# Kernel tuning notes

Hardware: AMD Instinct MI355X
Metric: run time of the kernel (lower is better)

Reference implementation:

```python
import jax, jax.numpy as jnp
import numpy as np

N = 10000
E = 320000
D_IN = 256
D_OUT = 256
EPS = 0.2  # initial value of trainable eps


def setup_inputs() -> dict:
    key = jax.random.key(0)
    ks = jax.random.split(key, 7)
    x = jax.random.normal(ks[0], (N, D_IN), dtype=jnp.float32)
    edge_index = jax.random.randint(ks[1], (2, E), 0, N, dtype=jnp.int64)
    # MLP params (Linear(in,out) -> ReLU -> Linear(out,out)), Kaiming-ish scale
    w1 = jax.random.normal(ks[2], (D_IN, D_OUT), dtype=jnp.float32) / np.sqrt(D_IN)
    b1 = jnp.zeros((D_OUT,), dtype=jnp.float32)
    w2 = jax.random.normal(ks[3], (D_OUT, D_OUT), dtype=jnp.float32) / np.sqrt(D_OUT)
    b2 = jnp.zeros((D_OUT,), dtype=jnp.float32)
    eps = jnp.float32(EPS)
    return {"x": x, "edge_index": edge_index, "w1": w1, "b1": b1,
            "w2": w2, "b2": b2, "eps": eps}


def reference(x, edge_index, w1, b1, w2, b2, eps):
    src, dst = edge_index[0], edge_index[1]
    # GIN sum aggregation: agg[i] = sum_{(j->i) in E} x[j]
    msgs = x[src]  # [E, D_IN] gather
    agg = jax.ops.segment_sum(msgs, dst, num_segments=N)  # [N, D_IN] scatter-add
    h = (1.0 + eps) * x + agg
    # 2-layer MLP
    h = jax.nn.relu(h @ w1 + b1)
    out = h @ w2 + b2
    return out
```

## Files before the change

kernel.cpp:

```cpp
#include <hip/hip_runtime.h>

#define NN 10000
#define NE 320000
#define CAP 96

typedef __bf16 bf16x8 __attribute__((ext_vector_type(8)));
typedef float f32x4 __attribute__((ext_vector_type(4)));
typedef unsigned short us8 __attribute__((ext_vector_type(8)));

static __device__ __forceinline__ unsigned short f2bf(float f) {
  union { float fv; unsigned u; } v; v.fv = f;
  unsigned r = v.u + 0x7FFFu + ((v.u >> 16) & 1u);
  return (unsigned short)(r >> 16);
}
static __device__ __forceinline__ float bf2f(unsigned short b) {
  union { unsigned u; float f; } v; v.u = ((unsigned)b) << 16;
  return v.f;
}


__global__ __launch_bounds__(256) void conv_k(const float* __restrict__ x,
                                              const float* __restrict__ w1,
                                              const float* __restrict__ w2,
                                              ushort4* __restrict__ xb4,
                                              unsigned short* __restrict__ w1t,
                                              unsigned short* __restrict__ w2t,
                                              int* __restrict__ cnt) {
  __shared__ unsigned short sh[64][72];
  int bid = blockIdx.x, tid = threadIdx.x;
  if (bid < 2500) {
    int t = bid * 256 + tid;
    if (t < 10240) cnt[t] = 0;
    float4 v = reinterpret_cast<const float4*>(x)[t];
    ushort4 o;
    o.x = f2bf(v.x); o.y = f2bf(v.y); o.z = f2bf(v.z); o.w = f2bf(v.w);
    xb4[t] = o;
  } else {
    int b2 = bid - 2500;
    const float* w = (b2 & 16) ? w2 : w1;
    unsigned short* wt = (b2 & 16) ? w2t : w1t;
    int tile = b2 & 15;
    int ki0 = (tile >> 2) * 64, ni0 = (tile & 3) * 64;
    int r = tid >> 4, c = tid & 15;
#pragma unroll
    for (int rr = r; rr < 64; rr += 16) {
      float4 v = *reinterpret_cast<const float4*>(&w[(ki0 + rr) * 256 + ni0 + c * 4]);
      ushort4 o;
      o.x = f2bf(v.x); o.y = f2bf(v.y); o.z = f2bf(v.z); o.w = f2bf(v.w);
      *reinterpret_cast<ushort4*>(&sh[rr][c * 4]) = o;
    }
    __syncthreads();
    int n = tid >> 3, c8 = tid & 7;
#pragma unroll
    for (int nn = n; nn < 64; nn += 32) {
      us8 o;
#pragma unroll
      for (int j = 0; j < 8; ++j) o[j] = sh[c8 * 8 + j][nn];
      *reinterpret_cast<us8*>(&wt[(ni0 + nn) * 256 + ki0 + c8 * 8]) = o;
    }
  }
}


__global__ __launch_bounds__(256) void fill_k(const int* __restrict__ ei,
                                              int* __restrict__ cnt,
                                              int* __restrict__ bucket) {
  int e = (blockIdx.x * 256 + threadIdx.x) * 4;
  if (e < NE) {
    int4 s = *reinterpret_cast<const int4*>(&ei[e]);
    int4 d = *reinterpret_cast<const int4*>(&ei[NE + e]);
    int p;
    p = atomicAdd(&cnt[d.x], 1); if (p < CAP) bucket[d.x * CAP + p] = s.x;
    p = atomicAdd(&cnt[d.y], 1); if (p < CAP) bucket[d.y * CAP + p] = s.y;
    p = atomicAdd(&cnt[d.z], 1); if (p < CAP) bucket[d.z * CAP + p] = s.z;
    p = atomicAdd(&cnt[d.w], 1); if (p < CAP) bucket[d.w * CAP + p] = s.w;
  }
}


__global__ __launch_bounds__(256) void agg_k(const us8* __restrict__ xb8,
                                             const int* __restrict__ cnt,
                                             const int* __restrict__ bucket,
                                             const float* __restrict__ epsp,
                                             unsigned short* __restrict__ hb) {
  __shared__ float part[2][256];
  int tid = threadIdx.x;
  int wave = tid >> 6;
  int slot = wave >> 1;
  int p = wave & 1;
  int node = blockIdx.x * 2 + slot;
  int lane = tid & 63;
  int half = lane >> 5, off = lane & 31;
  float e1 = 1.0f + epsp[0];

  float a[8];
  if (p == 0) {
    us8 sv = xb8[node * 32 + off];
    float selfw = half ? 0.0f : e1;
#pragma unroll
    for (int j = 0; j < 8; ++j) a[j] = bf2f(sv[j]) * selfw;
  } else {
#pragma unroll
    for (int j = 0; j < 8; ++j) a[j] = 0.0f;
  }

  int n = min(cnt[node], CAP);
  int n0 = ((n + 4) >> 3) << 2;
  int s = p ? n0 : 0;
  int m = (p ? n : n0) - s;
  const int4* bp4 = reinterpret_cast<const int4*>(bucket + node * CAP + s);
  int4 ia = bp4[0], ib = bp4[1];
  int k = 0;
  while (k + 8 <= m) {
    int4 na = bp4[(k >> 2) + 2];
    int4 nb = bp4[(k >> 2) + 3];
    int r0 = half ? ia.y : ia.x;
    int r1 = half ? ia.w : ia.z;
    int r2 = half ? ib.y : ib.x;
    int r3 = half ? ib.w : ib.z;
    us8 v0 = xb8[r0 * 32 + off];
    us8 v1 = xb8[r1 * 32 + off];
    us8 v2 = xb8[r2 * 32 + off];
    us8 v3 = xb8[r3 * 32 + off];
#pragma unroll
    for (int j = 0; j < 8; ++j)
      a[j] += (bf2f(v0[j]) + bf2f(v1[j])) + (bf2f(v2[j]) + bf2f(v3[j]));
    ia = na; ib = nb; k += 8;
  }
  int tl = m - k;
#pragma unroll
  for (int q = 0; q < 4; ++q) {
    int idx = (q == 0) ? (half ? ia.y : ia.x)
            : (q == 1) ? (half ? ia.w : ia.z)
            : (q == 2) ? (half ? ib.y : ib.x)
                       : (half ? ib.w : ib.z);
    if (2 * q + half < tl) {
      us8 v = xb8[idx * 32 + off];
#pragma unroll
      for (int j = 0; j < 8; ++j) a[j] += bf2f(v[j]);
    }
  }
#pragma unroll
  for (int j = 0; j < 8; ++j) a[j] += __shfl_xor(a[j], 32);
  if (p == 1 && half == 0) {
#pragma unroll
    for (int j = 0; j < 8; ++j) part[slot][j * 32 + off] = a[j];
  }
  __syncthreads();
  if (p == 0 && half == 0) {
    us8 o;
#pragma unroll
    for (int j = 0; j < 8; ++j) o[j] = f2bf(a[j] + part[slot][j * 32 + off]);
    *reinterpret_cast<us8*>(&hb[node * 256 + off * 8]) = o;
  }
}


__global__ __launch_bounds__(256) void mlp_k(const unsigned short* __restrict__ hb,
                                             const unsigned short* __restrict__ w1t,
                                             const float* __restrict__ b1,
                                             const unsigned short* __restrict__ w2t,
                                             const float* __restrict__ b2,
                                             float* __restrict__ out) {
  __shared__ unsigned short As[32][264];
  __shared__ unsigned short Bs[256][72];
  int m0 = blockIdx.x * 32;
  int tid = threadIdx.x;
  int lane = tid & 63, wave = tid >> 6;
  int waveM = wave & 1, waveN = wave >> 1;
  int l15 = lane & 15, g = lane >> 4;
#pragma unroll
  for (int i = 0; i < 4; ++i) {
    int c = tid + i * 256;
    int r = c >> 5, cc = c & 31;
    int4 v = (m0 + r < NN)
                 ? *reinterpret_cast<const int4*>(&hb[(m0 + r) * 256 + cc * 8])
                 : make_int4(0, 0, 0, 0);
    *reinterpret_cast<int4*>(&As[r][cc * 8]) = v;
  }
  float bias1[8], bias2[8];
#pragma unroll
  for (int ni = 0; ni < 8; ++ni) {
    int col = waveN * 128 + ni * 16 + l15;
    bias1[ni] = b1[col];
    bias2[ni] = b2[col];
  }
  f32x4 acc[8];
#pragma unroll
  for (int ni = 0; ni < 8; ++ni) acc[ni] = f32x4{0.f, 0.f, 0.f, 0.f};
  for (int k0 = 0; k0 < 256; k0 += 64) {
#pragma unroll
    for (int i = 0; i < 8; ++i) {
      int c = tid + i * 256;
      int n = c >> 3, kc = c & 7;
      *reinterpret_cast<int4*>(&Bs[n][kc * 8]) =
          *reinterpret_cast<const int4*>(&w1t[n * 256 + k0 + kc * 8]);
    }
    __syncthreads();
#pragma unroll
    for (int kk = 0; kk < 2; ++kk) {
      bf16x8 af = *reinterpret_cast<const bf16x8*>(
          &As[waveM * 16 + l15][k0 + kk * 32 + g * 8]);
#pragma unroll
      for (int ni = 0; ni < 8; ++ni) {
        bf16x8 bfr = *reinterpret_cast<const bf16x8*>(
            &Bs[waveN * 128 + ni * 16 + l15][kk * 32 + g * 8]);
        acc[ni] = __builtin_amdgcn_mfma_f32_16x16x32_bf16(af, bfr, acc[ni], 0, 0, 0);
      }
    }
    __syncthreads();
  }
#pragma unroll
  for (int ni = 0; ni < 8; ++ni) {
    int col = waveN * 128 + ni * 16 + l15;
#pragma unroll
    for (int r = 0; r < 4; ++r) {
      int row = waveM * 16 + g * 4 + r;
      As[row][col] = f2bf(fmaxf(acc[ni][r] + bias1[ni], 0.f));
    }
    acc[ni] = f32x4{0.f, 0.f, 0.f, 0.f};
  }
  for (int k0 = 0; k0 < 256; k0 += 64) {
#pragma unroll
    for (int i = 0; i < 8; ++i) {
      int c = tid + i * 256;
      int n = c >> 3, kc = c & 7;
      *reinterpret_cast<int4*>(&Bs[n][kc * 8]) =
          *reinterpret_cast<const int4*>(&w2t[n * 256 + k0 + kc * 8]);
    }
    __syncthreads();
#pragma unroll
    for (int kk = 0; kk < 2; ++kk) {
      bf16x8 af = *reinterpret_cast<const bf16x8*>(
          &As[waveM * 16 + l15][k0 + kk * 32 + g * 8]);
#pragma unroll
      for (int ni = 0; ni < 8; ++ni) {
        bf16x8 bfr = *reinterpret_cast<const bf16x8*>(
            &Bs[waveN * 128 + ni * 16 + l15][kk * 32 + g * 8]);
        acc[ni] = __builtin_amdgcn_mfma_f32_16x16x32_bf16(af, bfr, acc[ni], 0, 0, 0);
      }
    }
    __syncthreads();
  }
#pragma unroll
  for (int ni = 0; ni < 8; ++ni) {
    int col = waveN * 128 + ni * 16 + l15;
#pragma unroll
    for (int r = 0; r < 4; ++r) {
      int row = m0 + waveM * 16 + g * 4 + r;
      if (row < NN) out[row * 256 + col] = acc[ni][r] + bias2[ni];
    }
  }
}


extern "C" void kernel_launch(void* const* d_in, const int* in_sizes, int n_in,
                              void* d_out, int out_size, void* d_ws, size_t ws_size,
                              hipStream_t stream) {
  const float* x = (const float*)d_in[0];
  const int* ei = (const int*)d_in[1];
  const float* w1 = (const float*)d_in[2];
  const float* b1 = (const float*)d_in[3];
  const float* w2 = (const float*)d_in[4];
  const float* b2 = (const float*)d_in[5];
  const float* eps = (const float*)d_in[6];
  float* out = (float*)d_out;

  int* cnt = (int*)d_ws;
  int* bucket = cnt + 10240;
  unsigned short* xb = (unsigned short*)(bucket + NN * CAP + 32);
  unsigned short* w1t = xb + NN * 256;
  unsigned short* w2t = w1t + 65536;
  unsigned short* hb = w2t + 65536;

  conv_k<<<2532, 256, 0, stream>>>(x, w1, w2, (ushort4*)xb, w1t, w2t, cnt);
  fill_k<<<(NE / 4 + 255) / 256, 256, 0, stream>>>(ei, cnt, bucket);
  agg_k<<<NN / 2, 256, 0, stream>>>((const us8*)xb, cnt, bucket, eps, hb);
  mlp_k<<<(NN + 31) / 32, 256, 0, stream>>>(hb, w1t, b1, w2t, b2, out);
}
```

Before: 64.07 us.

## Fuse conversion and bucket fill into one prep kernel, deepen gather unroll

Merges the x/weight bf16 conversion kernel and the edge-bucket fill kernel into a single grid-stride prep kernel. The count array is now zeroed with a memset issued before it. This removes one kernel launch and lets the atomic fill overlap with the conversion traffic. The aggregation loop now issues 8 neighbour gathers per iteration instead of 4 to keep more loads in flight, with a wider tail and larger bucket padding. The trade-offs are an extra memset launch and more registers per thread in the aggregation kernel.

```diff
diff --git a/kernel.cpp b/kernel.cpp
--- a/kernel.cpp
+++ b/kernel.cpp
@@ -3,6 +3,8 @@
 #define NN 10000
 #define NE 320000
 #define CAP 96
+#define K1BLK 1024
+#define K1TOT (K1BLK * 256)
 
 typedef __bf16 bf16x8 __attribute__((ext_vector_type(8)));
 typedef float f32x4 __attribute__((ext_vector_type(4)));
@@ -19,54 +21,21 @@
 }
 
 
-__global__ __launch_bounds__(256) void conv_k(const float* __restrict__ x,
+__global__ __launch_bounds__(256) void prep_k(const float* __restrict__ x,
+                                              const int* __restrict__ ei,
                                               const float* __restrict__ w1,
                                               const float* __restrict__ w2,
                                               ushort4* __restrict__ xb4,
                                               unsigned short* __restrict__ w1t,
                                               unsigned short* __restrict__ w2t,
-                                              int* __restrict__ cnt) {
+                                              int* __restrict__ cnt,
+                                              int* __restrict__ bucket) {
   __shared__ unsigned short sh[64][72];
   int bid = blockIdx.x, tid = threadIdx.x;
-  if (bid < 2500) {
-    int t = bid * 256 + tid;
-    if (t < 10240) cnt[t] = 0;
-    float4 v = reinterpret_cast<const float4*>(x)[t];
-    ushort4 o;
-    o.x = f2bf(v.x); o.y = f2bf(v.y); o.z = f2bf(v.z); o.w = f2bf(v.w);
-    xb4[t] = o;
-  } else {
-    int b2 = bid - 2500;
-    const float* w = (b2 & 16) ? w2 : w1;
-    unsigned short* wt = (b2 & 16) ? w2t : w1t;
-    int tile = b2 & 15;
-    int ki0 = (tile >> 2) * 64, ni0 = (tile & 3) * 64;
-    int r = tid >> 4, c = tid & 15;
-#pragma unroll
-    for (int rr = r; rr < 64; rr += 16) {
-      float4 v = *reinterpret_cast<const float4*>(&w[(ki0 + rr) * 256 + ni0 + c * 4]);
-      ushort4 o;
-      o.x = f2bf(v.x); o.y = f2bf(v.y); o.z = f2bf(v.z); o.w = f2bf(v.w);
-      *reinterpret_cast<ushort4*>(&sh[rr][c * 4]) = o;
-    }
-    __syncthreads();
-    int n = tid >> 3, c8 = tid & 7;
-#pragma unroll
-    for (int nn = n; nn < 64; nn += 32) {
-      us8 o;
-#pragma unroll
-      for (int j = 0; j < 8; ++j) o[j] = sh[c8 * 8 + j][nn];
-      *reinterpret_cast<us8*>(&wt[(ni0 + nn) * 256 + ki0 + c8 * 8]) = o;
-    }
-  }
-}
-
-
-__global__ __launch_bounds__(256) void fill_k(const int* __restrict__ ei,
-                                              int* __restrict__ cnt,
-                                              int* __restrict__ bucket) {
-  int e = (blockIdx.x * 256 + threadIdx.x) * 4;
-  if (e < NE) {
+  int gtid = bid * 256 + tid;
+
+  if (gtid < NE / 4) {
+    int e = gtid * 4;
     int4 s = *reinterpret_cast<const int4*>(&ei[e]);
     int4 d = *reinterpret_cast<const int4*>(&ei[NE + e]);
     int p;
@@ -74,6 +43,38 @@
     p = atomicAdd(&cnt[d.y], 1); if (p < CAP) bucket[d.y * CAP + p] = s.y;
     p = atomicAdd(&cnt[d.z], 1); if (p < CAP) bucket[d.z * CAP + p] = s.z;
     p = atomicAdd(&cnt[d.w], 1); if (p < CAP) bucket[d.w * CAP + p] = s.w;
+  }
+
+  for (int t = gtid; t < 640000; t += K1TOT) {
+    float4 v = reinterpret_cast<const float4*>(x)[t];
+    ushort4 o;
+    o.x = f2bf(v.x); o.y = f2bf(v.y); o.z = f2bf(v.z); o.w = f2bf(v.w);
+    xb4[t] = o;
+  }
+
+  if (bid >= 512 && bid < 544) {
+    int b2 = bid - 512;
+    const float* w = (b2 & 16) ? w2 : w1;
+    unsigned short* wt = (b2 & 16) ? w2t : w1t;
+    int tile = b2 & 15;
+    int ki0 = (tile >> 2) * 64, ni0 = (tile & 3) * 64;
+    int r = tid >> 4, c = tid & 15;
+#pragma unroll
+    for (int rr = r; rr < 64; rr += 16) {
+      float4 v = *reinterpret_cast<const float4*>(&w[(ki0 + rr) * 256 + ni0 + c * 4]);
+      ushort4 o;
+      o.x = f2bf(v.x); o.y = f2bf(v.y); o.z = f2bf(v.z); o.w = f2bf(v.w);
+      *reinterpret_cast<ushort4*>(&sh[rr][c * 4]) = o;
+    }
+    __syncthreads();
+    int n = tid >> 3, c8 = tid & 7;
+#pragma unroll
+    for (int nn = n; nn < 64; nn += 32) {
+      us8 o;
+#pragma unroll
+      for (int j = 0; j < 8; ++j) o[j] = sh[c8 * 8 + j][nn];
+      *reinterpret_cast<us8*>(&wt[(ni0 + nn) * 256 + ki0 + c8 * 8]) = o;
+    }
   }
 }
 
@@ -109,36 +110,44 @@
   int s = p ? n0 : 0;
   int m = (p ? n : n0) - s;
   const int4* bp4 = reinterpret_cast<const int4*>(bucket + node * CAP + s);
-  int4 ia = bp4[0], ib = bp4[1];
+  int4 ia = bp4[0], ib = bp4[1], ic = bp4[2], id = bp4[3];
   int k = 0;
-  while (k + 8 <= m) {
-    int4 na = bp4[(k >> 2) + 2];
-    int4 nb = bp4[(k >> 2) + 3];
-    int r0 = half ? ia.y : ia.x;
-    int r1 = half ? ia.w : ia.z;
-    int r2 = half ? ib.y : ib.x;
-    int r3 = half ? ib.w : ib.z;
+  while (k + 16 <= m) {
+    int base = (k >> 2) + 4;
+    int4 na = bp4[base], nb = bp4[base + 1];
+    int4 nc = bp4[base + 2], nd = bp4[base + 3];
+    int r0 = half ? ia.y : ia.x, r1 = half ? ia.w : ia.z;
+    int r2 = half ? ib.y : ib.x, r3 = half ? ib.w : ib.z;
+    int r4 = half ? ic.y : ic.x, r5 = half ? ic.w : ic.z;
+    int r6 = half ? id.y : id.x, r7 = half ? id.w : id.z;
     us8 v0 = xb8[r0 * 32 + off];
     us8 v1 = xb8[r1 * 32 + off];
     us8 v2 = xb8[r2 * 32 + off];
     us8 v3 = xb8[r3 * 32 + off];
+    us8 v4 = xb8[r4 * 32 + off];
+    us8 v5 = xb8[r5 * 32 + off];
+    us8 v6 = xb8[r6 * 32 + off];
+    us8 v7 = xb8[r7 * 32 + off];
 #pragma unroll
     for (int j = 0; j < 8; ++j)
-      a[j] += (bf2f(v0[j]) + bf2f(v1[j])) + (bf2f(v2[j]) + bf2f(v3[j]));
-    ia = na; ib = nb; k += 8;
+      a[j] += ((bf2f(v0[j]) + bf2f(v1[j])) + (bf2f(v2[j]) + bf2f(v3[j]))) +
+              ((bf2f(v4[j]) + bf2f(v5[j])) + (bf2f(v6[j]) + bf2f(v7[j])));
+    ia = na; ib = nb; ic = nc; id = nd; k += 16;
   }
   int tl = m - k;
-#pragma unroll
-  for (int q = 0; q < 4; ++q) {
-    int idx = (q == 0) ? (half ? ia.y : ia.x)
-            : (q == 1) ? (half ? ia.w : ia.z)
-            : (q == 2) ? (half ? ib.y : ib.x)
-                       : (half ? ib.w : ib.z);
-    if (2 * q + half < tl) {
-      us8 v = xb8[idx * 32 + off];
-#pragma unroll
-      for (int j = 0; j < 8; ++j) a[j] += bf2f(v[j]);
-    }
+  {
+    int r0 = half ? ia.y : ia.x, r1 = half ? ia.w : ia.z;
+    int r2 = half ? ib.y : ib.x, r3 = half ? ib.w : ib.z;
+    int r4 = half ? ic.y : ic.x, r5 = half ? ic.w : ic.z;
+    int r6 = half ? id.y : id.x, r7 = half ? id.w : id.z;
+#define TAILQ(q, rq)                                        \
+    if (2 * q + half < tl) {                                \
+      us8 v = xb8[rq * 32 + off];                           \
+      _Pragma("unroll") for (int j = 0; j < 8; ++j) a[j] += bf2f(v[j]); \
+    }
+    TAILQ(0, r0) TAILQ(1, r1) TAILQ(2, r2) TAILQ(3, r3)
+    TAILQ(4, r4) TAILQ(5, r5) TAILQ(6, r6) TAILQ(7, r7)
+#undef TAILQ
   }
 #pragma unroll
   for (int j = 0; j < 8; ++j) a[j] += __shfl_xor(a[j], 32);
@@ -268,13 +277,14 @@
 
   int* cnt = (int*)d_ws;
   int* bucket = cnt + 10240;
-  unsigned short* xb = (unsigned short*)(bucket + NN * CAP + 32);
+  unsigned short* xb = (unsigned short*)(bucket + NN * CAP + 64);
   unsigned short* w1t = xb + NN * 256;
   unsigned short* w2t = w1t + 65536;
   unsigned short* hb = w2t + 65536;
 
-  conv_k<<<2532, 256, 0, stream>>>(x, w1, w2, (ushort4*)xb, w1t, w2t, cnt);
-  fill_k<<<(NE / 4 + 255) / 256, 256, 0, stream>>>(ei, cnt, bucket);
+  hipMemsetAsync(cnt, 0, 10240 * sizeof(int), stream);
+  prep_k<<<K1BLK, 256, 0, stream>>>(x, ei, w1, w2, (ushort4*)xb, w1t, w2t,
+                                    cnt, bucket);
   agg_k<<<NN / 2, 256, 0, stream>>>((const us8*)xb, cnt, bucket, eps, hb);
   mlp_k<<<(NN + 31) / 32, 256, 0, stream>>>(hb, w1t, b1, w2t, b2, out);
 }
```

Result: slower. 71.41 us (+11.5%).

## Fuse neighbor aggregation into MLP kernel with 1024-thread blocks and register-prefetched weights

Applied to the files above, without the earlier changes.

Merges the aggregation and MLP kernels into one 1024-thread kernel. Each of the 16 waves aggregates two node rows straight into the shared A tile, so the bf16 intermediate h no longer goes through global memory and one launch is dropped. The MLP is split across 16 waves, each computing a 16x32 output tile, and the next weight chunk is prefetched into registers while the current chunk's MFMAs run. The cost is that aggregation now uses one wave per node instead of two, so per-node parallelism drops and degree imbalance inside a block can stall the GEMM phase. The large blocks also limit occupancy and scheduling flexibility.

```diff
diff --git a/kernel.cpp b/kernel.cpp
--- a/kernel.cpp
+++ b/kernel.cpp
@@ -78,173 +78,156 @@
 }
 
 
-__global__ __launch_bounds__(256) void agg_k(const us8* __restrict__ xb8,
-                                             const int* __restrict__ cnt,
-                                             const int* __restrict__ bucket,
-                                             const float* __restrict__ epsp,
-                                             unsigned short* __restrict__ hb) {
-  __shared__ float part[2][256];
-  int tid = threadIdx.x;
-  int wave = tid >> 6;
-  int slot = wave >> 1;
-  int p = wave & 1;
-  int node = blockIdx.x * 2 + slot;
-  int lane = tid & 63;
-  int half = lane >> 5, off = lane & 31;
-  float e1 = 1.0f + epsp[0];
-
-  float a[8];
-  if (p == 0) {
-    us8 sv = xb8[node * 32 + off];
-    float selfw = half ? 0.0f : e1;
-#pragma unroll
-    for (int j = 0; j < 8; ++j) a[j] = bf2f(sv[j]) * selfw;
-  } else {
-#pragma unroll
-    for (int j = 0; j < 8; ++j) a[j] = 0.0f;
-  }
-
-  int n = min(cnt[node], CAP);
-  int n0 = ((n + 4) >> 3) << 2;
-  int s = p ? n0 : 0;
-  int m = (p ? n : n0) - s;
-  const int4* bp4 = reinterpret_cast<const int4*>(bucket + node * CAP + s);
-  int4 ia = bp4[0], ib = bp4[1];
-  int k = 0;
-  while (k + 8 <= m) {
-    int4 na = bp4[(k >> 2) + 2];
-    int4 nb = bp4[(k >> 2) + 3];
-    int r0 = half ? ia.y : ia.x;
-    int r1 = half ? ia.w : ia.z;
-    int r2 = half ? ib.y : ib.x;
-    int r3 = half ? ib.w : ib.z;
-    us8 v0 = xb8[r0 * 32 + off];
-    us8 v1 = xb8[r1 * 32 + off];
-    us8 v2 = xb8[r2 * 32 + off];
-    us8 v3 = xb8[r3 * 32 + off];
-#pragma unroll
-    for (int j = 0; j < 8; ++j)
-      a[j] += (bf2f(v0[j]) + bf2f(v1[j])) + (bf2f(v2[j]) + bf2f(v3[j]));
-    ia = na; ib = nb; k += 8;
-  }
-  int tl = m - k;
-#pragma unroll
-  for (int q = 0; q < 4; ++q) {
-    int idx = (q == 0) ? (half ? ia.y : ia.x)
-            : (q == 1) ? (half ? ia.w : ia.z)
-            : (q == 2) ? (half ? ib.y : ib.x)
-                       : (half ? ib.w : ib.z);
-    if (2 * q + half < tl) {
-      us8 v = xb8[idx * 32 + off];
-#pragma unroll
-      for (int j = 0; j < 8; ++j) a[j] += bf2f(v[j]);
-    }
-  }
-#pragma unroll
-  for (int j = 0; j < 8; ++j) a[j] += __shfl_xor(a[j], 32);
-  if (p == 1 && half == 0) {
-#pragma unroll
-    for (int j = 0; j < 8; ++j) part[slot][j * 32 + off] = a[j];
-  }
-  __syncthreads();
-  if (p == 0 && half == 0) {
-    us8 o;
-#pragma unroll
-    for (int j = 0; j < 8; ++j) o[j] = f2bf(a[j] + part[slot][j * 32 + off]);
-    *reinterpret_cast<us8*>(&hb[node * 256 + off * 8]) = o;
-  }
-}
-
-
-__global__ __launch_bounds__(256) void mlp_k(const unsigned short* __restrict__ hb,
-                                             const unsigned short* __restrict__ w1t,
-                                             const float* __restrict__ b1,
-                                             const unsigned short* __restrict__ w2t,
-                                             const float* __restrict__ b2,
-                                             float* __restrict__ out) {
+__global__ __launch_bounds__(1024, 4) void fused_k(
+    const us8* __restrict__ xb8, const int* __restrict__ cnt,
+    const int* __restrict__ bucket, const float* __restrict__ epsp,
+    const unsigned short* __restrict__ w1t, const float* __restrict__ b1,
+    const unsigned short* __restrict__ w2t, const float* __restrict__ b2,
+    float* __restrict__ out) {
   __shared__ unsigned short As[32][264];
   __shared__ unsigned short Bs[256][72];
   int m0 = blockIdx.x * 32;
-  int tid = threadIdx.x;
-  int lane = tid & 63, wave = tid >> 6;
+  int tid = threadIdx.x, lane = tid & 63, wave = tid >> 6;
+  int half = lane >> 5, off = lane & 31;
+  float e1 = 1.0f + epsp[0];
+
+#pragma unroll
+  for (int which = 0; which < 2; ++which) {
+    int row = wave * 2 + which;
+    int node = m0 + row;
+    float a[8];
+    if (node < NN) {
+      us8 sv = xb8[node * 32 + off];
+      float selfw = half ? 0.0f : e1;
+#pragma unroll
+      for (int j = 0; j < 8; ++j) a[j] = bf2f(sv[j]) * selfw;
+      int n = min(cnt[node], CAP);
+      const int4* bp4 = reinterpret_cast<const int4*>(bucket + node * CAP);
+      int4 ia = bp4[0], ib = bp4[1];
+      int k = 0;
+      while (k + 8 <= n) {
+        int4 na = bp4[(k >> 2) + 2];
+        int4 nb = bp4[(k >> 2) + 3];
+        int r0 = half ? ia.y : ia.x;
+        int r1 = half ? ia.w : ia.z;
+        int r2 = half ? ib.y : ib.x;
+        int r3 = half ? ib.w : ib.z;
+        us8 v0 = xb8[r0 * 32 + off];
+        us8 v1 = xb8[r1 * 32 + off];
+        us8 v2 = xb8[r2 * 32 + off];
+        us8 v3 = xb8[r3 * 32 + off];
+#pragma unroll
+        for (int j = 0; j < 8; ++j)
+          a[j] += (bf2f(v0[j]) + bf2f(v1[j])) + (bf2f(v2[j]) + bf2f(v3[j]));
+        ia = na; ib = nb; k += 8;
+      }
+      int tl = n - k;
+#pragma unroll
+      for (int q = 0; q < 4; ++q) {
+        int idx = (q == 0) ? (half ? ia.y : ia.x)
+                : (q == 1) ? (half ? ia.w : ia.z)
+                : (q == 2) ? (half ? ib.y : ib.x)
+                           : (half ? ib.w : ib.z);
+        if (2 * q + half < tl) {
+          us8 v = xb8[idx * 32 + off];
+#pragma unroll
+          for (int j = 0; j < 8; ++j) a[j] += bf2f(v[j]);
+        }
+      }
+#pragma unroll
+      for (int j = 0; j < 8; ++j) a[j] += __shfl_xor(a[j], 32);
+    } else {
+#pragma unroll
+      for (int j = 0; j < 8; ++j) a[j] = 0.0f;
+    }
+    if (half == 0) {
+      us8 o;
+#pragma unroll
+      for (int j = 0; j < 8; ++j) o[j] = f2bf(a[j]);
+      *reinterpret_cast<us8*>(&As[row][off * 8]) = o;
+    }
+  }
+
   int waveM = wave & 1, waveN = wave >> 1;
   int l15 = lane & 15, g = lane >> 4;
-#pragma unroll
-  for (int i = 0; i < 4; ++i) {
-    int c = tid + i * 256;
-    int r = c >> 5, cc = c & 31;
-    int4 v = (m0 + r < NN)
-                 ? *reinterpret_cast<const int4*>(&hb[(m0 + r) * 256 + cc * 8])
-                 : make_int4(0, 0, 0, 0);
-    *reinterpret_cast<int4*>(&As[r][cc * 8]) = v;
-  }
-  float bias1[8], bias2[8];
-#pragma unroll
-  for (int ni = 0; ni < 8; ++ni) {
-    int col = waveN * 128 + ni * 16 + l15;
+  float bias1[2], bias2[2];
+#pragma unroll
+  for (int ni = 0; ni < 2; ++ni) {
+    int col = waveN * 32 + ni * 16 + l15;
     bias1[ni] = b1[col];
     bias2[ni] = b2[col];
   }
-  f32x4 acc[8];
-#pragma unroll
-  for (int ni = 0; ni < 8; ++ni) acc[ni] = f32x4{0.f, 0.f, 0.f, 0.f};
-  for (int k0 = 0; k0 < 256; k0 += 64) {
-#pragma unroll
-    for (int i = 0; i < 8; ++i) {
-      int c = tid + i * 256;
-      int n = c >> 3, kc = c & 7;
-      *reinterpret_cast<int4*>(&Bs[n][kc * 8]) =
-          *reinterpret_cast<const int4*>(&w1t[n * 256 + k0 + kc * 8]);
-    }
-    __syncthreads();
+
+  int4 rv[2];
+#pragma unroll
+  for (int i = 0; i < 2; ++i) {
+    int c = tid + i * 1024;
+    int n = c >> 3, kc = c & 7;
+    rv[i] = *reinterpret_cast<const int4*>(&w1t[n * 256 + kc * 8]);
+  }
+#pragma unroll
+  for (int i = 0; i < 2; ++i) {
+    int c = tid + i * 1024;
+    int n = c >> 3, kc = c & 7;
+    *reinterpret_cast<int4*>(&Bs[n][kc * 8]) = rv[i];
+  }
+  __syncthreads();
+
+  f32x4 acc[2];
+  acc[0] = f32x4{0.f, 0.f, 0.f, 0.f};
+  acc[1] = f32x4{0.f, 0.f, 0.f, 0.f};
+
+#pragma unroll
+  for (int cc2 = 0; cc2 < 8; ++cc2) {
+    int k0 = (cc2 & 3) * 64;
+    if (cc2 < 7) {
+      const unsigned short* wt = (cc2 + 1 < 4) ? w1t : w2t;
+      int kn = ((cc2 + 1) & 3) * 64;
+#pragma unroll
+      for (int i = 0; i < 2; ++i) {
+        int c = tid + i * 1024;
+        int n = c >> 3, kc = c & 7;
+        rv[i] = *reinterpret_cast<const int4*>(&wt[n * 256 + kn + kc * 8]);
+      }
+    }
 #pragma unroll
     for (int kk = 0; kk < 2; ++kk) {
       bf16x8 af = *reinterpret_cast<const bf16x8*>(
           &As[waveM * 16 + l15][k0 + kk * 32 + g * 8]);
 #pragma unroll
-      for (int ni = 0; ni < 8; ++ni) {
+      for (int ni = 0; ni < 2; ++ni) {
         bf16x8 bfr = *reinterpret_cast<const bf16x8*>(
-            &Bs[waveN * 128 + ni * 16 + l15][kk * 32 + g * 8]);
+            &Bs[waveN * 32 + ni * 16 + l15][kk * 32 + g * 8]);
         acc[ni] = __builtin_amdgcn_mfma_f32_16x16x32_bf16(af, bfr, acc[ni], 0, 0, 0);
       }
     }
-    __syncthreads();
-  }
-#pragma unroll
-  for (int ni = 0; ni < 8; ++ni) {
-    int col = waveN * 128 + ni * 16 + l15;
-#pragma unroll
-    for (int r = 0; r < 4; ++r) {
-      int row = waveM * 16 + g * 4 + r;
-      As[row][col] = f2bf(fmaxf(acc[ni][r] + bias1[ni], 0.f));
-    }
-    acc[ni] = f32x4{0.f, 0.f, 0.f, 0.f};
-  }
-  for (int k0 = 0; k0 < 256; k0 += 64) {
-#pragma unroll
-    for (int i = 0; i < 8; ++i) {
-      int c = tid + i * 256;
-      int n = c >> 3, kc = c & 7;
-      *reinterpret_cast<int4*>(&Bs[n][kc * 8]) =
-          *reinterpret_cast<const int4*>(&w2t[n * 256 + k0 + kc * 8]);
-    }
-    __syncthreads();
-#pragma unroll
-    for (int kk = 0; kk < 2; ++kk) {
-      bf16x8 af = *reinterpret_cast<const bf16x8*>(
-          &As[waveM * 16 + l15][k0 + kk * 32 + g * 8]);
-#pragma unroll
-      for (int ni = 0; ni < 8; ++ni) {
-        bf16x8 bfr = *reinterpret_cast<const bf16x8*>(
-            &Bs[waveN * 128 + ni * 16 + l15][kk * 32 + g * 8]);
-        acc[ni] = __builtin_amdgcn_mfma_f32_16x16x32_bf16(af, bfr, acc[ni], 0, 0, 0);
-      }
-    }
-    __syncthreads();
-  }
-#pragma unroll
-  for (int ni = 0; ni < 8; ++ni) {
-    int col = waveN * 128 + ni * 16 + l15;
+    if (cc2 < 7) {
+      __syncthreads();
+      if (cc2 == 3) {
+#pragma unroll
+        for (int ni = 0; ni < 2; ++ni) {
+          int col = waveN * 32 + ni * 16 + l15;
+#pragma unroll
+          for (int r = 0; r < 4; ++r) {
+            int row = waveM * 16 + g * 4 + r;
+            As[row][col] = f2bf(fmaxf(acc[ni][r] + bias1[ni], 0.f));
+          }
+          acc[ni] = f32x4{0.f, 0.f, 0.f, 0.f};
+        }
+      }
+#pragma unroll
+      for (int i = 0; i < 2; ++i) {
+        int c = tid + i * 1024;
+        int n = c >> 3, kc = c & 7;
+        *reinterpret_cast<int4*>(&Bs[n][kc * 8]) = rv[i];
+      }
+      __syncthreads();
+    }
+  }
+
+#pragma unroll
+  for (int ni = 0; ni < 2; ++ni) {
+    int col = waveN * 32 + ni * 16 + l15;
 #pragma unroll
     for (int r = 0; r < 4; ++r) {
       int row = m0 + waveM * 16 + g * 4 + r;
@@ -271,10 +254,9 @@
   unsigned short* xb = (unsigned short*)(bucket + NN * CAP + 32);
   unsigned short* w1t = xb + NN * 256;
   unsigned short* w2t = w1t + 65536;
-  unsigned short* hb = w2t + 65536;
 
   conv_k<<<2532, 256, 0, stream>>>(x, w1, w2, (ushort4*)xb, w1t, w2t, cnt);
   fill_k<<<(NE / 4 + 255) / 256, 256, 0, stream>>>(ei, cnt, bucket);
-  agg_k<<<NN / 2, 256, 0, stream>>>((const us8*)xb, cnt, bucket, eps, hb);
-  mlp_k<<<(NN + 31) / 32, 256, 0, stream>>>(hb, w1t, b1, w2t, b2, out);
-}
+  fused_k<<<(NN + 31) / 32, 1024, 0, stream>>>((const us8*)xb, cnt, bucket, eps,
+                                               w1t, b1, w2t, b2, out);
+}
```

Result: slower. 88.44 us (+38.0%).
